# Optimization experiments

Hardware: AMD Instinct MI355X
Metric: run time of the kernel (lower is better)

The kernel has to match this reference:

```python
import jax, jax.numpy as jnp
import numpy as np

EPS = 1e-5

def _act_quant(x):
    # per-token int8 absmax quantization (BitNet b1.58)
    scale = 127.0 / jnp.clip(jnp.max(jnp.abs(x), axis=-1, keepdims=True), EPS)
    return jnp.clip(jnp.round(x * scale), -128.0, 127.0) / scale

def _weight_quant(w):
    # per-tensor ternary quantization: round(w/mean|w|) clipped to {-1,0,1}
    scale = 1.0 / jnp.clip(jnp.mean(jnp.abs(w)), EPS)
    return jnp.clip(jnp.round(w * scale), -1.0, 1.0) / scale

def _ste(x, q):
    # straight-through estimator: forward uses q, backward passes through x
    return x + jax.lax.stop_gradient(q - x)

def bitlinear(x, w):
    xq = _ste(x, _act_quant(x))
    wq = _ste(w, _weight_quant(w))
    return jnp.einsum('btd,hd->bth', xq, wq)

def setup_inputs() -> dict:
    key = jax.random.key(0)
    k1, k2, k3 = jax.random.split(key, 3)
    B, T, D, H = 4, 1024, 2048, 8192
    x = jax.random.normal(k1, (B, T, D), dtype=jnp.float32)
    w1 = jax.random.normal(k2, (H, D), dtype=jnp.float32) * 0.02
    w2 = jax.random.normal(k3, (D, H), dtype=jnp.float32) * 0.02
    return {"x": x, "w1": w1, "w2": w2}

def reference(x, w1, w2):
    h = jax.nn.relu(bitlinear(x, w1))   # [B, T, H]
    out = bitlinear(h, w2)              # [B, T, D]
    return out
```

## Files before the change

### kernel.cpp

```cpp
#include <hip/hip_runtime.h>
#include <hip/hip_bf16.h>

#define EPSF 1e-5f

typedef int v4i __attribute__((ext_vector_type(4)));
typedef int v16i __attribute__((ext_vector_type(16)));
typedef short v8s __attribute__((ext_vector_type(8)));

static constexpr int BB = 4, TT = 1024, DD = 2048, HH = 8192;
static constexpr int MROWS = BB * TT;
static constexpr long long WCOUNT = (long long)DD * HH;


__device__ __forceinline__ void async_copy16(const void* g, void* l) {
  __builtin_amdgcn_global_load_lds(
      (const __attribute__((address_space(1))) unsigned int*)g,
      (__attribute__((address_space(3))) unsigned int*)l,
      16, 0, 0);
}

__device__ __forceinline__ int pack4(float a, float b, float c, float d,
                                     float scale, float lo, float hi) {
  int ia = (int)fminf(fmaxf(rintf(a * scale), lo), hi);
  int ib = (int)fminf(fmaxf(rintf(b * scale), lo), hi);
  int ic = (int)fminf(fmaxf(rintf(c * scale), lo), hi);
  int id = (int)fminf(fmaxf(rintf(d * scale), lo), hi);
  return (ia & 0xff) | ((ib & 0xff) << 8) | ((ic & 0xff) << 16) | ((id & 0xff) << 24);
}

__device__ __forceinline__ float abs4(float4 v) {
  return fmaxf(fmaxf(fabsf(v.x), fabsf(v.y)), fmaxf(fabsf(v.z), fabsf(v.w)));
}

__device__ __forceinline__ int blockMaxI256(int v) {
  #pragma unroll
  for (int off = 32; off; off >>= 1) v = max(v, __shfl_down(v, off, 64));
  __shared__ int sm[4];
  int lane = threadIdx.x & 63, wv = threadIdx.x >> 6;
  if (lane == 0) sm[wv] = v;
  __syncthreads();
  return max(max(sm[0], sm[1]), max(sm[2], sm[3]));
}

__device__ __forceinline__ void swizzle_tiles(int& mt, int& nt) {
  int Mt = gridDim.y, Nt = gridDim.x;
  int id = blockIdx.y * Nt + blockIdx.x;
  int c = id & 7, k = id >> 3;
  int pm = (Mt >= Nt) ? 4 : 2;
  int PM = Mt / pm, PN = Nt / (8 / pm);
  int pr = c % pm, pc = c / pm;
  mt = pr * PM + (k % PM);
  nt = pc * PN + (k / PM);
}


__global__ __launch_bounds__(256) void prep_kernel(
    const float* __restrict__ w1, const float* __restrict__ w2,
    const float* __restrict__ x, float* __restrict__ partials,
    signed char* __restrict__ xq, float* __restrict__ ascale) {
  __shared__ float sm[4];
  const int bid = blockIdx.x, t = threadIdx.x;
  const int lane = t & 63, wv = t >> 6;

  if (bid < 4096) {
    const int y = bid >> 11, b = bid & 2047;
    const float4* w4 = (const float4*)(y ? w2 : w1);
    const long long base = (long long)b * 2048;
    float4 u[8];
    #pragma unroll
    for (int k = 0; k < 8; k++) u[k] = w4[base + t + k * 256];
    float s = 0.f;
    #pragma unroll
    for (int k = 0; k < 8; k++)
      s += fabsf(u[k].x) + fabsf(u[k].y) + fabsf(u[k].z) + fabsf(u[k].w);
    #pragma unroll
    for (int off = 32; off; off >>= 1) s += __shfl_down(s, off, 64);
    if (lane == 0) sm[wv] = s;
    __syncthreads();
    if (t == 0) partials[y * 2048 + b] = sm[0] + sm[1] + sm[2] + sm[3];
  } else {
    int row = (bid - 4096) * 4 + wv;
    const float4* xr = (const float4*)(x + (size_t)row * DD);
    float4 v[8];
    #pragma unroll
    for (int j = 0; j < 8; j++) v[j] = xr[lane + j * 64];
    float m = 0.f;
    #pragma unroll
    for (int j = 0; j < 8; j++) m = fmaxf(m, abs4(v[j]));
    #pragma unroll
    for (int off = 32; off; off >>= 1) m = fmaxf(m, __shfl_down(m, off, 64));
    m = __shfl(m, 0, 64);
    float am = fmaxf(m, EPSF);
    float scale = 127.0f / am;
    int* out = (int*)(xq + (size_t)row * DD);
    #pragma unroll
    for (int j = 0; j < 8; j++)
      out[lane + j * 64] = pack4(v[j].x, v[j].y, v[j].z, v[j].w, scale, -128.f, 127.f);
    if (lane == 0) ascale[row] = am / 127.0f;
  }
}


__global__ __launch_bounds__(256) void quant_w_kernel(
    const float* __restrict__ w1, const float* __restrict__ w2,
    const float* __restrict__ partials, float* __restrict__ meanw,
    signed char* __restrict__ q1, signed char* __restrict__ q2) {
  const int y = blockIdx.y, bid = blockIdx.x, t = threadIdx.x;
  const int lane = t & 63, wv = t >> 6;

  double d = 0.0;
  #pragma unroll
  for (int j = 0; j < 8; j++) d += (double)partials[y * 2048 + t + j * 256];
  #pragma unroll
  for (int off = 32; off; off >>= 1) d += __shfl_down(d, off, 64);
  __shared__ double smd[4];
  if (lane == 0) smd[wv] = d;
  __syncthreads();
  double sum = smd[0] + smd[1] + smd[2] + smd[3];
  float mean = fmaxf((float)(sum * (1.0 / (double)WCOUNT)), EPSF);
  if (bid == 0 && t == 0) meanw[y] = mean;
  float sc = 1.0f / mean;

  const float4* w4 = (const float4*)(y ? w2 : w1);
  int* q4 = (int*)(y ? q2 : q1);
  const long long base = (long long)bid * 2048;
  float4 u[8];
  #pragma unroll
  for (int k = 0; k < 8; k++) u[k] = w4[base + t + k * 256];
  #pragma unroll
  for (int k = 0; k < 8; k++)
    q4[base + t + k * 256] = pack4(u[k].x, u[k].y, u[k].z, u[k].w, sc, -1.f, 1.f);
}


__global__ __launch_bounds__(256) void quant_h_kernel(
    const short* __restrict__ h, signed char* __restrict__ hq,
    float* __restrict__ a2, const float* __restrict__ a1,
    const float* __restrict__ meanw) {
  int row = blockIdx.x;
  int t = threadIdx.x;
  const v8s* hr = (const v8s*)(h + (size_t)row * HH);
  v8s v[4];
  #pragma unroll
  for (int i = 0; i < 4; i++) v[i] = hr[t + i * 256];
  int mx = 0;
  #pragma unroll
  for (int i = 0; i < 4; i++)
    #pragma unroll
    for (int j = 0; j < 8; j++) mx = max(mx, (int)v[i][j]);
  int bmx = blockMaxI256(mx);
  float f = a1[row] * meanw[0];
  float maxh = (float)bmx * f;
  float am = fmaxf(maxh, EPSF);
  float scale = 127.0f / am;
  int2* out = (int2*)(hq + (size_t)row * HH);
  #pragma unroll
  for (int i = 0; i < 4; i++) {
    int p0 = pack4((float)v[i][0] * f, (float)v[i][1] * f, (float)v[i][2] * f,
                   (float)v[i][3] * f, scale, -128.f, 127.f);
    int p1 = pack4((float)v[i][4] * f, (float)v[i][5] * f, (float)v[i][6] * f,
                   (float)v[i][7] * f, scale, -128.f, 127.f);
    out[t + i * 256] = int2{p0, p1};
  }
  if (t == 0) a2[row] = am / 127.0f;
}


template <int MODE, int BK>
__global__ __launch_bounds__(256) void gemm_i8_kernel(
    const signed char* __restrict__ A, const signed char* __restrict__ B,
    void* __restrict__ Cout, const float* __restrict__ ascale,
    const float* __restrict__ wmean_p, int M, int N, int K) {
  constexpr int CH = BK / 16;
  constexpr int SEGROWS = 1024 / BK;
  constexpr int SPW = BK / 32;
  __shared__ signed char As[128 * BK];
  __shared__ signed char Bs[128 * BK];

  const int t = threadIdx.x;
  const int lane = t & 63, wv = t >> 6;
  const int wm = wv >> 1, wn = wv & 1;
  int mt, nt;
  swizzle_tiles(mt, nt);
  const int m0 = mt * 128, n0 = nt * 128;
  const int hf = lane >> 5;

  const signed char* aSrc[SPW];
  const signed char* bSrc[SPW];
  #pragma unroll
  for (int i = 0; i < SPW; i++) {
    int seg = wv * SPW + i;
    int r = seg * SEGROWS + lane / CH;
    int c = (lane % CH) ^ (r & (CH - 1));
    aSrc[i] = A + (size_t)(m0 + r) * K + c * 16;
    bSrc[i] = B + (size_t)(n0 + r) * K + c * 16;
  }

  v16i acc[2][2];
  #pragma unroll
  for (int i = 0; i < 2; i++)
    #pragma unroll
    for (int j = 0; j < 2; j++) {
      v16i z = {0, 0, 0, 0, 0, 0, 0, 0, 0, 0, 0, 0, 0, 0, 0, 0};
      acc[i][j] = z;
    }

  int rowA[2], rowB[2];
  #pragma unroll
  for (int i = 0; i < 2; i++) {
    rowA[i] = wm * 64 + i * 32 + (lane & 31);
    rowB[i] = wn * 64 + i * 32 + (lane & 31);
  }

  for (int k0 = 0; k0 < K; k0 += BK) {
    #pragma unroll
    for (int i = 0; i < SPW; i++) {
      async_copy16(aSrc[i] + k0, &As[(wv * SPW + i) * 1024]);
      async_copy16(bSrc[i] + k0, &Bs[(wv * SPW + i) * 1024]);
    }
    __syncthreads();
    #pragma unroll
    for (int ks = 0; ks < BK / 32; ks++) {
      v4i af[2], bf[2];
      #pragma unroll
      for (int i = 0; i < 2; i++) {
        int ca = (ks * 2 + hf) ^ (rowA[i] & (CH - 1));
        af[i] = *(const v4i*)(As + rowA[i] * BK + ca * 16);
        int cb = (ks * 2 + hf) ^ (rowB[i] & (CH - 1));
        bf[i] = *(const v4i*)(Bs + rowB[i] * BK + cb * 16);
      }
      #pragma unroll
      for (int i = 0; i < 2; i++)
        #pragma unroll
        for (int j = 0; j < 2; j++)
          acc[i][j] = __builtin_amdgcn_mfma_i32_32x32x32_i8(af[i], bf[j], acc[i][j], 0, 0, 0);
    }
    __syncthreads();
  }

  if constexpr (MODE == 1) {
    short* C = (short*)Cout;
    #pragma unroll
    for (int i = 0; i < 2; i++) {
      #pragma unroll
      for (int e = 0; e < 16; e++) {
        int m = m0 + wm * 64 + i * 32 + (e & 3) + 8 * (e >> 2) + 4 * hf;
        #pragma unroll
        for (int j = 0; j < 2; j++) {
          int n = n0 + wn * 64 + j * 32 + (lane & 31);
          int r = acc[i][j][e];
          r = r < 0 ? 0 : (r > 32767 ? 32767 : r);
          C[(size_t)m * N + n] = (short)r;
        }
      }
    }
  } else {
    float* C = (float*)Cout;
    float wmean = wmean_p[0];
    #pragma unroll
    for (int i = 0; i < 2; i++) {
      #pragma unroll
      for (int e = 0; e < 16; e++) {
        int m = m0 + wm * 64 + i * 32 + (e & 3) + 8 * (e >> 2) + 4 * hf;
        float f = ascale[m] * wmean;
        #pragma unroll
        for (int j = 0; j < 2; j++) {
          int n = n0 + wn * 64 + j * 32 + (lane & 31);
          C[(size_t)m * N + n] = (float)acc[i][j][e] * f;
        }
      }
    }
  }
}


extern "C" void kernel_launch(void* const* d_in, const int* in_sizes, int n_in,
                              void* d_out, int out_size, void* d_ws, size_t ws_size,
                              hipStream_t stream) {
  const float* x  = (const float*)d_in[0];
  const float* w1 = (const float*)d_in[1];
  const float* w2 = (const float*)d_in[2];
  float* out = (float*)d_out;

  char* ws = (char*)d_ws;
  float* meanw = (float*)ws;
  float* partials = (float*)(ws + 1024);
  float* a1 = (float*)(ws + 20480);
  float* a2 = (float*)(ws + 40960);
  signed char* w1q = (signed char*)(ws + 65536);
  signed char* w2q = w1q + (size_t)WCOUNT;
  signed char* xq  = w2q + (size_t)WCOUNT;
  signed char* hq  = xq + (size_t)MROWS * DD;
  short* h16 = (short*)(hq + (size_t)MROWS * HH);

  prep_kernel<<<5120, 256, 0, stream>>>(w1, w2, x, partials, xq, a1);
  quant_w_kernel<<<dim3(2048, 2), 256, 0, stream>>>(w1, w2, partials, meanw, w1q, w2q);
  gemm_i8_kernel<1, 128><<<dim3(HH / 128, MROWS / 128), 256, 0, stream>>>(
      xq, w1q, h16, nullptr, meanw, MROWS, HH, DD);
  quant_h_kernel<<<MROWS, 256, 0, stream>>>(h16, hq, a2, a1, meanw);
  gemm_i8_kernel<0, 256><<<dim3(DD / 128, MROWS / 128), 256, 0, stream>>>(
      hq, w2q, out, a2, &meanw[1], MROWS, DD, HH);
}
```

Measured before the change: 373.6 us.

## Double-buffer LDS tiles in int8 GEMM with a smaller K step

Both int8 MFMA GEMMs now use two LDS buffers with a fixed BK of 64, instead of a single buffer with BK of 128 or 256. The async global-to-LDS copy for the next K tile is issued before the MFMAs on the current tile, so loads can overlap compute. Launch bounds now ask for 4 blocks per CU to raise occupancy. The smaller K step doubles or quadruples the number of loop iterations and barriers, and gives less MFMA work per load to hide latency behind.

```diff
diff --git a/kernel.cpp b/kernel.cpp
--- a/kernel.cpp
+++ b/kernel.cpp
@@ -166,16 +166,17 @@
 }
 
 
-template <int MODE, int BK>
-__global__ __launch_bounds__(256) void gemm_i8_kernel(
+template <int MODE>
+__global__ __launch_bounds__(256, 4) void gemm_i8_kernel(
     const signed char* __restrict__ A, const signed char* __restrict__ B,
     void* __restrict__ Cout, const float* __restrict__ ascale,
     const float* __restrict__ wmean_p, int M, int N, int K) {
+  constexpr int BK = 64;
   constexpr int CH = BK / 16;
   constexpr int SEGROWS = 1024 / BK;
   constexpr int SPW = BK / 32;
-  __shared__ signed char As[128 * BK];
-  __shared__ signed char Bs[128 * BK];
+  __shared__ signed char As[2][128 * BK];
+  __shared__ signed char Bs[2][128 * BK];
 
   const int t = threadIdx.x;
   const int lane = t & 63, wv = t >> 6;
@@ -212,22 +213,31 @@
     rowB[i] = wn * 64 + i * 32 + (lane & 31);
   }
 
-  for (int k0 = 0; k0 < K; k0 += BK) {
+  auto stage = [&](int kt, int bu) {
     #pragma unroll
     for (int i = 0; i < SPW; i++) {
-      async_copy16(aSrc[i] + k0, &As[(wv * SPW + i) * 1024]);
-      async_copy16(bSrc[i] + k0, &Bs[(wv * SPW + i) * 1024]);
-    }
-    __syncthreads();
+      async_copy16(aSrc[i] + (size_t)kt * BK, &As[bu][(wv * SPW + i) * 1024]);
+      async_copy16(bSrc[i] + (size_t)kt * BK, &Bs[bu][(wv * SPW + i) * 1024]);
+    }
+  };
+
+  const int NK = K / BK;
+  stage(0, 0);
+  __syncthreads();
+
+  for (int kt = 0; kt < NK; ++kt) {
+    if (kt + 1 < NK) stage(kt + 1, (kt + 1) & 1);
+    const signed char* as_ = As[kt & 1];
+    const signed char* bs_ = Bs[kt & 1];
     #pragma unroll
     for (int ks = 0; ks < BK / 32; ks++) {
       v4i af[2], bf[2];
       #pragma unroll
       for (int i = 0; i < 2; i++) {
         int ca = (ks * 2 + hf) ^ (rowA[i] & (CH - 1));
-        af[i] = *(const v4i*)(As + rowA[i] * BK + ca * 16);
+        af[i] = *(const v4i*)(as_ + rowA[i] * BK + ca * 16);
         int cb = (ks * 2 + hf) ^ (rowB[i] & (CH - 1));
-        bf[i] = *(const v4i*)(Bs + rowB[i] * BK + cb * 16);
+        bf[i] = *(const v4i*)(bs_ + rowB[i] * BK + cb * 16);
       }
       #pragma unroll
       for (int i = 0; i < 2; i++)
@@ -295,9 +305,9 @@
 
   prep_kernel<<<5120, 256, 0, stream>>>(w1, w2, x, partials, xq, a1);
   quant_w_kernel<<<dim3(2048, 2), 256, 0, stream>>>(w1, w2, partials, meanw, w1q, w2q);
-  gemm_i8_kernel<1, 128><<<dim3(HH / 128, MROWS / 128), 256, 0, stream>>>(
+  gemm_i8_kernel<1><<<dim3(HH / 128, MROWS / 128), 256, 0, stream>>>(
       xq, w1q, h16, nullptr, meanw, MROWS, HH, DD);
   quant_h_kernel<<<MROWS, 256, 0, stream>>>(h16, hq, a2, a1, meanw);
-  gemm_i8_kernel<0, 256><<<dim3(DD / 128, MROWS / 128), 256, 0, stream>>>(
+  gemm_i8_kernel<0><<<dim3(DD / 128, MROWS / 128), 256, 0, stream>>>(
       hq, w2q, out, a2, &meanw[1], MROWS, DD, HH);
 }
```

New measurement: 420.1 us. 1.12x slower.

## Enlarge GEMM tiles to 256x128 and fuse per-row max of h into GEMM1 epilogue

Applied to the files above, without the earlier changes.

Both int8 GEMMs now use 256x128 tiles with four 32-row fragments per wave, and both are launched with occupancy hint 2. The second GEMM also drops from BK=256 to BK=128. This raises MFMA work per LDS load and halves the grid in M. The first GEMM's epilogue computes the per-row max of the clamped output and writes it with atomicMax into a buffer that the prep kernel zeroes. This removes the max pass and block reduction from quant_h, at the cost of more registers, atomic traffic, and a buffer (a2) that holds int row maxima before being overwritten with float scales.

```diff
diff --git a/kernel.cpp b/kernel.cpp
--- a/kernel.cpp
+++ b/kernel.cpp
@@ -30,16 +30,6 @@
 
 __device__ __forceinline__ float abs4(float4 v) {
   return fmaxf(fmaxf(fabsf(v.x), fabsf(v.y)), fmaxf(fabsf(v.z), fabsf(v.w)));
-}
-
-__device__ __forceinline__ int blockMaxI256(int v) {
-  #pragma unroll
-  for (int off = 32; off; off >>= 1) v = max(v, __shfl_down(v, off, 64));
-  __shared__ int sm[4];
-  int lane = threadIdx.x & 63, wv = threadIdx.x >> 6;
-  if (lane == 0) sm[wv] = v;
-  __syncthreads();
-  return max(max(sm[0], sm[1]), max(sm[2], sm[3]));
 }
 
 __device__ __forceinline__ void swizzle_tiles(int& mt, int& nt) {
@@ -57,7 +47,8 @@
 __global__ __launch_bounds__(256) void prep_kernel(
     const float* __restrict__ w1, const float* __restrict__ w2,
     const float* __restrict__ x, float* __restrict__ partials,
-    signed char* __restrict__ xq, float* __restrict__ ascale) {
+    signed char* __restrict__ xq, float* __restrict__ ascale,
+    int* __restrict__ rowMax) {
   __shared__ float sm[4];
   const int bid = blockIdx.x, t = threadIdx.x;
   const int lane = t & 63, wv = t >> 6;
@@ -78,7 +69,7 @@
     if (lane == 0) sm[wv] = s;
     __syncthreads();
     if (t == 0) partials[y * 2048 + b] = sm[0] + sm[1] + sm[2] + sm[3];
-  } else {
+  } else if (bid < 5120) {
     int row = (bid - 4096) * 4 + wv;
     const float4* xr = (const float4*)(x + (size_t)row * DD);
     float4 v[8];
@@ -97,6 +88,8 @@
     for (int j = 0; j < 8; j++)
       out[lane + j * 64] = pack4(v[j].x, v[j].y, v[j].z, v[j].w, scale, -128.f, 127.f);
     if (lane == 0) ascale[row] = am / 127.0f;
+  } else {
+    rowMax[(bid - 5120) * 256 + t] = 0;
   }
 }
 
@@ -135,24 +128,21 @@
 
 __global__ __launch_bounds__(256) void quant_h_kernel(
     const short* __restrict__ h, signed char* __restrict__ hq,
-    float* __restrict__ a2, const float* __restrict__ a1,
+    float* __restrict__ a2_rowmax, const float* __restrict__ a1,
     const float* __restrict__ meanw) {
   int row = blockIdx.x;
   int t = threadIdx.x;
+  int bmx = ((const int*)a2_rowmax)[row];
   const v8s* hr = (const v8s*)(h + (size_t)row * HH);
   v8s v[4];
   #pragma unroll
   for (int i = 0; i < 4; i++) v[i] = hr[t + i * 256];
-  int mx = 0;
-  #pragma unroll
-  for (int i = 0; i < 4; i++)
-    #pragma unroll
-    for (int j = 0; j < 8; j++) mx = max(mx, (int)v[i][j]);
-  int bmx = blockMaxI256(mx);
   float f = a1[row] * meanw[0];
   float maxh = (float)bmx * f;
   float am = fmaxf(maxh, EPSF);
   float scale = 127.0f / am;
+  __syncthreads();
+  if (t == 0) a2_rowmax[row] = am / 127.0f;
   int2* out = (int2*)(hq + (size_t)row * HH);
   #pragma unroll
   for (int i = 0; i < 4; i++) {
@@ -162,75 +152,86 @@
                    (float)v[i][7] * f, scale, -128.f, 127.f);
     out[t + i * 256] = int2{p0, p1};
   }
-  if (t == 0) a2[row] = am / 127.0f;
-}
-
-
-template <int MODE, int BK>
-__global__ __launch_bounds__(256) void gemm_i8_kernel(
+}
+
+
+template <int MODE>
+__device__ __forceinline__ void gemm_body(
     const signed char* __restrict__ A, const signed char* __restrict__ B,
     void* __restrict__ Cout, const float* __restrict__ ascale,
-    const float* __restrict__ wmean_p, int M, int N, int K) {
+    const float* __restrict__ wmean_p, int* __restrict__ rowMax,
+    int M, int N, int K) {
+  constexpr int BM = 256, BN = 128, BK = 128;
   constexpr int CH = BK / 16;
-  constexpr int SEGROWS = 1024 / BK;
-  constexpr int SPW = BK / 32;
-  __shared__ signed char As[128 * BK];
-  __shared__ signed char Bs[128 * BK];
+  constexpr int SEGR = 1024 / BK;
+  constexpr int SPA = (BM * BK / 1024) / 4;
+  constexpr int SPB = (BN * BK / 1024) / 4;
+  __shared__ signed char As[BM * BK];
+  __shared__ signed char Bs[BN * BK];
 
   const int t = threadIdx.x;
   const int lane = t & 63, wv = t >> 6;
   const int wm = wv >> 1, wn = wv & 1;
   int mt, nt;
   swizzle_tiles(mt, nt);
-  const int m0 = mt * 128, n0 = nt * 128;
+  const int m0 = mt * BM, n0 = nt * BN;
   const int hf = lane >> 5;
 
-  const signed char* aSrc[SPW];
-  const signed char* bSrc[SPW];
-  #pragma unroll
-  for (int i = 0; i < SPW; i++) {
-    int seg = wv * SPW + i;
-    int r = seg * SEGROWS + lane / CH;
+  const signed char* aSrc[SPA];
+  const signed char* bSrc[SPB];
+  #pragma unroll
+  for (int i = 0; i < SPA; i++) {
+    int seg = wv * SPA + i;
+    int r = seg * SEGR + lane / CH;
     int c = (lane % CH) ^ (r & (CH - 1));
     aSrc[i] = A + (size_t)(m0 + r) * K + c * 16;
+  }
+  #pragma unroll
+  for (int i = 0; i < SPB; i++) {
+    int seg = wv * SPB + i;
+    int r = seg * SEGR + lane / CH;
+    int c = (lane % CH) ^ (r & (CH - 1));
     bSrc[i] = B + (size_t)(n0 + r) * K + c * 16;
   }
 
-  v16i acc[2][2];
-  #pragma unroll
-  for (int i = 0; i < 2; i++)
+  v16i acc[4][2];
+  #pragma unroll
+  for (int i = 0; i < 4; i++)
     #pragma unroll
     for (int j = 0; j < 2; j++) {
       v16i z = {0, 0, 0, 0, 0, 0, 0, 0, 0, 0, 0, 0, 0, 0, 0, 0};
       acc[i][j] = z;
     }
 
-  int rowA[2], rowB[2];
-  #pragma unroll
-  for (int i = 0; i < 2; i++) {
-    rowA[i] = wm * 64 + i * 32 + (lane & 31);
-    rowB[i] = wn * 64 + i * 32 + (lane & 31);
-  }
+  int rowA[4], rowB[2];
+  #pragma unroll
+  for (int i = 0; i < 4; i++) rowA[i] = wm * 128 + i * 32 + (lane & 31);
+  #pragma unroll
+  for (int j = 0; j < 2; j++) rowB[j] = wn * 64 + j * 32 + (lane & 31);
 
   for (int k0 = 0; k0 < K; k0 += BK) {
     #pragma unroll
-    for (int i = 0; i < SPW; i++) {
-      async_copy16(aSrc[i] + k0, &As[(wv * SPW + i) * 1024]);
-      async_copy16(bSrc[i] + k0, &Bs[(wv * SPW + i) * 1024]);
-    }
+    for (int i = 0; i < SPA; i++)
+      async_copy16(aSrc[i] + k0, &As[(wv * SPA + i) * 1024]);
+    #pragma unroll
+    for (int i = 0; i < SPB; i++)
+      async_copy16(bSrc[i] + k0, &Bs[(wv * SPB + i) * 1024]);
     __syncthreads();
     #pragma unroll
     for (int ks = 0; ks < BK / 32; ks++) {
-      v4i af[2], bf[2];
-      #pragma unroll
-      for (int i = 0; i < 2; i++) {
+      v4i af[4], bf[2];
+      #pragma unroll
+      for (int j = 0; j < 2; j++) {
+        int cb = (ks * 2 + hf) ^ (rowB[j] & (CH - 1));
+        bf[j] = *(const v4i*)(Bs + rowB[j] * BK + cb * 16);
+      }
+      #pragma unroll
+      for (int i = 0; i < 4; i++) {
         int ca = (ks * 2 + hf) ^ (rowA[i] & (CH - 1));
         af[i] = *(const v4i*)(As + rowA[i] * BK + ca * 16);
-        int cb = (ks * 2 + hf) ^ (rowB[i] & (CH - 1));
-        bf[i] = *(const v4i*)(Bs + rowB[i] * BK + cb * 16);
       }
       #pragma unroll
-      for (int i = 0; i < 2; i++)
+      for (int i = 0; i < 4; i++)
         #pragma unroll
         for (int j = 0; j < 2; j++)
           acc[i][j] = __builtin_amdgcn_mfma_i32_32x32x32_i8(af[i], bf[j], acc[i][j], 0, 0, 0);
@@ -241,27 +242,32 @@
   if constexpr (MODE == 1) {
     short* C = (short*)Cout;
     #pragma unroll
-    for (int i = 0; i < 2; i++) {
+    for (int i = 0; i < 4; i++) {
       #pragma unroll
       for (int e = 0; e < 16; e++) {
-        int m = m0 + wm * 64 + i * 32 + (e & 3) + 8 * (e >> 2) + 4 * hf;
+        int m = m0 + wm * 128 + i * 32 + (e & 3) + 8 * (e >> 2) + 4 * hf;
+        int rm = 0;
         #pragma unroll
         for (int j = 0; j < 2; j++) {
           int n = n0 + wn * 64 + j * 32 + (lane & 31);
           int r = acc[i][j][e];
           r = r < 0 ? 0 : (r > 32767 ? 32767 : r);
           C[(size_t)m * N + n] = (short)r;
+          rm = max(rm, r);
         }
+        #pragma unroll
+        for (int off = 16; off; off >>= 1) rm = max(rm, __shfl_xor(rm, off, 64));
+        if ((lane & 31) == 0) atomicMax(&rowMax[m], rm);
       }
     }
   } else {
     float* C = (float*)Cout;
     float wmean = wmean_p[0];
     #pragma unroll
-    for (int i = 0; i < 2; i++) {
+    for (int i = 0; i < 4; i++) {
       #pragma unroll
       for (int e = 0; e < 16; e++) {
-        int m = m0 + wm * 64 + i * 32 + (e & 3) + 8 * (e >> 2) + 4 * hf;
+        int m = m0 + wm * 128 + i * 32 + (e & 3) + 8 * (e >> 2) + 4 * hf;
         float f = ascale[m] * wmean;
         #pragma unroll
         for (int j = 0; j < 2; j++) {
@@ -271,6 +277,19 @@
       }
     }
   }
+}
+
+__global__ __launch_bounds__(256, 2) void gemm_relu_i8(
+    const signed char* __restrict__ A, const signed char* __restrict__ B,
+    short* __restrict__ C, int* __restrict__ rowMax, int M, int N, int K) {
+  gemm_body<1>(A, B, C, nullptr, nullptr, rowMax, M, N, K);
+}
+
+__global__ __launch_bounds__(256, 2) void gemm_out_i8(
+    const signed char* __restrict__ A, const signed char* __restrict__ B,
+    float* __restrict__ C, const float* __restrict__ ascale,
+    const float* __restrict__ wmean_p, int M, int N, int K) {
+  gemm_body<0>(A, B, C, ascale, wmean_p, nullptr, M, N, K);
 }
 
 
@@ -292,12 +311,13 @@
   signed char* xq  = w2q + (size_t)WCOUNT;
   signed char* hq  = xq + (size_t)MROWS * DD;
   short* h16 = (short*)(hq + (size_t)MROWS * HH);
-
-  prep_kernel<<<5120, 256, 0, stream>>>(w1, w2, x, partials, xq, a1);
+  int* rowMax = (int*)a2;
+
+  prep_kernel<<<5136, 256, 0, stream>>>(w1, w2, x, partials, xq, a1, rowMax);
   quant_w_kernel<<<dim3(2048, 2), 256, 0, stream>>>(w1, w2, partials, meanw, w1q, w2q);
-  gemm_i8_kernel<1, 128><<<dim3(HH / 128, MROWS / 128), 256, 0, stream>>>(
-      xq, w1q, h16, nullptr, meanw, MROWS, HH, DD);
+  gemm_relu_i8<<<dim3(HH / 128, MROWS / 256), 256, 0, stream>>>(
+      xq, w1q, h16, rowMax, MROWS, HH, DD);
   quant_h_kernel<<<MROWS, 256, 0, stream>>>(h16, hq, a2, a1, meanw);
-  gemm_i8_kernel<0, 256><<<dim3(DD / 128, MROWS / 128), 256, 0, stream>>>(
+  gemm_out_i8<<<dim3(DD / 128, MROWS / 256), 256, 0, stream>>>(
       hq, w2q, out, a2, &meanw[1], MROWS, DD, HH);
 }
```

Measured after the change: 426.7 us. +14.2%, slower.
